# Kernel optimization log

Hardware: AMD Instinct MI355X
Metric: run time of the kernel (lower is better)

The kernel has to match this reference:

```python
import jax, jax.numpy as jnp
import numpy as np

N_NODES = 100000

def _sage_conv(x, edge_index, w_l, b_l, w_r):
    # PyG SAGEConv (mean aggr): out = lin_l(mean_j x_j) + lin_r(x)
    src, dst = edge_index[0], edge_index[1]
    msgs = x[src]  # [E, F] gather
    agg = jax.ops.segment_sum(msgs, dst, num_segments=N_NODES)
    cnt = jax.ops.segment_sum(jnp.ones((edge_index.shape[1],), x.dtype), dst, num_segments=N_NODES)
    agg = agg / jnp.maximum(cnt, 1.0)[:, None]  # mean; isolated nodes -> 0
    return agg @ w_l.T + b_l + x @ w_r.T

def setup_inputs() -> dict:
    key = jax.random.key(0)
    k = jax.random.split(key, 8)
    in_c, hid, out_c = 128, 64, 32
    x = jax.random.normal(k[0], (N_NODES, in_c), dtype=jnp.float32)
    edge_index = jax.random.randint(k[1], (2, 600000), 0, N_NODES, dtype=jnp.int64)
    s = lambda kk, fo, fi: jax.random.normal(kk, (fo, fi), jnp.float32) / jnp.sqrt(fi)
    return {
        'x': x,
        'edge_index': edge_index,
        'w1_l': s(k[2], hid, in_c),
        'b1_l': jnp.zeros((hid,), jnp.float32),
        'w1_r': s(k[3], hid, in_c),
        'w2_l': s(k[4], out_c, hid),
        'b2_l': jnp.zeros((out_c,), jnp.float32),
        'w2_r': s(k[5], out_c, hid),
    }

def reference(x, edge_index, w1_l, b1_l, w1_r, w2_l, b2_l, w2_r):
    h = _sage_conv(x, edge_index, w1_l, b1_l, w1_r)
    h = jax.nn.relu(h)
    # dropout(p=0.3) is identity in eval mode
    return _sage_conv(h, edge_index, w2_l, b2_l, w2_r)
```

## Files before the change

### kernel.cpp

```cpp
#include <hip/hip_runtime.h>

#define N_NODES 100000
#define N_EDGES 600000
#define N_PAD   100352
#define CAP     40
#define G1_TILES 3125
#define G1_TPB   5
#define G1_BLOCKS 625
#define CSR_EPT 17
#define CSR_EPB (CSR_EPT * 256)
#define CSR_BLOCKS 138
#define FRONT_BLOCKS (G1_BLOCKS + CSR_BLOCKS)
#define MID_BLOCKS 3125

typedef __bf16 bf16x8 __attribute__((ext_vector_type(8)));
typedef float  f32x4  __attribute__((ext_vector_type(4)));
typedef unsigned short u16x8 __attribute__((ext_vector_type(8)));
typedef unsigned short u16x4 __attribute__((ext_vector_type(4)));

__device__ inline unsigned short f2bf(float f) {
    __bf16 h = (__bf16)f;
    return __builtin_bit_cast(unsigned short, h);
}
__device__ inline float bf2f(unsigned short u) {
    return __builtin_bit_cast(float, ((unsigned)u) << 16);
}
__device__ inline bf16x8 ldfrag_bf16(const unsigned short* p) {
    u16x8 v = *(const u16x8*)p;
    return __builtin_bit_cast(bf16x8, v);
}

__global__ __launch_bounds__(256) void prep(
    const float* __restrict__ w1l, const float* __restrict__ w1r,
    const float* __restrict__ w2l, const float* __restrict__ w2r,
    unsigned short* __restrict__ wbf1, unsigned short* __restrict__ wbf2,
    int* __restrict__ deg)
{
    int i = blockIdx.x * 256 + threadIdx.x;
    deg[i] = 0;
    if (i < 16384) {
        int row = i >> 7, k = i & 127;
        float v = (row < 64) ? w1l[(row << 7) + k] : w1r[((row - 64) << 7) + k];
        wbf1[i] = f2bf(v);
    } else if (i < 20480) {
        int j = i - 16384;
        int row = j >> 6, k = j & 63;
        float v = (row < 32) ? w2l[(row << 6) + k] : w2r[((row - 32) << 6) + k];
        wbf2[j] = f2bf(v);
    }
}

__global__ __launch_bounds__(256) void front(
    const float* __restrict__ x,
    const unsigned short* __restrict__ wbf1,
    const int* __restrict__ ei,
    unsigned short* __restrict__ xl,
    unsigned short* __restrict__ xr,
    int* __restrict__ deg,
    int* __restrict__ csr32)
{
    const int b   = blockIdx.x;
    const int tid = threadIdx.x;

    if (b >= G1_BLOCKS) {
        const int cb = b - G1_BLOCKS;
        const int e0 = cb * CSR_EPB + tid;
        int dst[CSR_EPT], src[CSR_EPT];
        #pragma unroll
        for (int rr = 0; rr < CSR_EPT; ++rr) {
            int e = e0 + rr * 256;
            if (e < N_EDGES) { dst[rr] = ei[N_EDGES + e]; src[rr] = ei[e]; }
            else             { dst[rr] = -1; }
        }
        #pragma unroll
        for (int rr = 0; rr < CSR_EPT; ++rr) {
            if (dst[rr] >= 0) {
                int pos = atomicAdd(&deg[dst[rr]], 1);
                if (pos < CAP) csr32[dst[rr] * CAP + pos] = src[rr];
            }
        }
        return;
    }

    __shared__ unsigned short wlds[128 * 128];
    __shared__ unsigned short xs[2][32 * 128];

    #pragma unroll
    for (int i = 0; i < 8; ++i) {
        int idx = i * 256 + tid;
        int row = idx >> 4;
        int off = (idx & 15) << 4;
        u16x8 v = *(const u16x8*)(wbf1 + row * 128 + (off >> 1));
        *(u16x8*)((char*)wlds + row * 256 + (off ^ ((row & 7) << 4))) = v;
    }

    const int t0 = b * G1_TPB;

    const int wv   = tid >> 6;
    const int l    = tid & 63;
    const int lrow = l & 15;
    const int hi   = l >> 4;
    const int sr0  = tid >> 4;
    const int soff = (tid & 15) << 4;

    float4 pf[4];

    #define SLOAD(t) do {                                                      \
        _Pragma("unroll")                                                      \
        for (int rr = 0; rr < 2; ++rr) {                                       \
            const float* src = x + (size_t)((t) * 32 + sr0 + rr * 16) * 128    \
                                 + (soff >> 1);                                \
            pf[2*rr]   = *(const float4*)src;                                  \
            pf[2*rr+1] = *(const float4*)(src + 4);                            \
        }                                                                      \
    } while (0)

    #define SWRITE(bf) do {                                                    \
        _Pragma("unroll")                                                      \
        for (int rr = 0; rr < 2; ++rr) {                                       \
            int row = sr0 + rr * 16;                                           \
            u16x8 o;                                                           \
            o[0]=f2bf(pf[2*rr].x);   o[1]=f2bf(pf[2*rr].y);                    \
            o[2]=f2bf(pf[2*rr].z);   o[3]=f2bf(pf[2*rr].w);                    \
            o[4]=f2bf(pf[2*rr+1].x); o[5]=f2bf(pf[2*rr+1].y);                  \
            o[6]=f2bf(pf[2*rr+1].z); o[7]=f2bf(pf[2*rr+1].w);                  \
            *(u16x8*)((char*)&xs[bf][0] + row * 256                            \
                      + (soff ^ ((row & 7) << 4))) = o;                        \
        }                                                                      \
    } while (0)

    SLOAD(t0);
    SWRITE(0);
    __syncthreads();

    for (int tt = 0; tt < G1_TPB; ++tt) {
        if (tt + 1 < G1_TPB) SLOAD(t0 + tt + 1);

        char* xb = (char*)&xs[tt & 1][0];
        f32x4 acc[2][2];
        #pragma unroll
        for (int nt = 0; nt < 2; ++nt)
            #pragma unroll
            for (int ft = 0; ft < 2; ++ft) acc[nt][ft] = (f32x4){0.f,0.f,0.f,0.f};

        #pragma unroll
        for (int kt = 0; kt < 4; ++kt) {
            const int koff = kt * 64 + hi * 16;
            const int r0 = lrow, r1 = 16 + lrow;
            bf16x8 b0 = __builtin_bit_cast(bf16x8, *(const u16x8*)
                (xb + r0 * 256 + (koff ^ ((r0 & 7) << 4))));
            bf16x8 b1 = __builtin_bit_cast(bf16x8, *(const u16x8*)
                (xb + r1 * 256 + (koff ^ ((r1 & 7) << 4))));
            #pragma unroll
            for (int ft = 0; ft < 2; ++ft) {
                const int fr = wv * 32 + ft * 16 + lrow;
                bf16x8 a = __builtin_bit_cast(bf16x8, *(const u16x8*)
                    ((char*)wlds + fr * 256 + (koff ^ ((fr & 7) << 4))));
                acc[0][ft] = __builtin_amdgcn_mfma_f32_16x16x32_bf16(a, b0, acc[0][ft], 0, 0, 0);
                acc[1][ft] = __builtin_amdgcn_mfma_f32_16x16x32_bf16(a, b1, acc[1][ft], 0, 0, 0);
            }
        }

        if (tt + 1 < G1_TPB) SWRITE((tt + 1) & 1);
        __syncthreads();

        #pragma unroll
        for (int nt = 0; nt < 2; ++nt) {
            const int node = nt * 16 + lrow;
            #pragma unroll
            for (int ft = 0; ft < 2; ++ft) {
                const int fb = (wv * 32 + ft * 16 + hi * 4) * 2;
                u16x4 p;
                p[0] = f2bf(acc[nt][ft][0]); p[1] = f2bf(acc[nt][ft][1]);
                p[2] = f2bf(acc[nt][ft][2]); p[3] = f2bf(acc[nt][ft][3]);
                *(u16x4*)(xb + node * 256 + (fb ^ ((node & 7) << 4))) = p;
            }
        }
        __syncthreads();

        const int nbase = (t0 + tt) * 32;
        #pragma unroll
        for (int rr = 0; rr < 2; ++rr) {
            int idx = rr * 256 + tid;
            int row = idx >> 4;
            int off = (idx & 15) << 4;
            u16x8 v = *(const u16x8*)(xb + row * 256 + (off ^ ((row & 7) << 4)));
            if (off < 128) *(u16x8*)&xl[(nbase + row) * 64 + (off >> 1)] = v;
            else           *(u16x8*)&xr[(nbase + row) * 64 + ((off - 128) >> 1)] = v;
        }
        __syncthreads();
    }
    #undef SLOAD
    #undef SWRITE
}

__global__ __launch_bounds__(256) void mid(
    const unsigned short* __restrict__ xl,
    const unsigned short* __restrict__ xr,
    const int* __restrict__ deg,
    const int* __restrict__ csr32,
    const float* __restrict__ b1l,
    const unsigned short* __restrict__ wbf2,
    unsigned short* __restrict__ hl,
    unsigned short* __restrict__ hr)
{
    __shared__ unsigned short hs[32 * 64];

    const int tid = threadIdx.x;
    const int nd  = tid >> 3;
    const int q   = tid & 7;
    const int node = blockIdx.x * 32 + nd;

    const int beg = node * CAP;
    const int dg  = min(deg[node], CAP);

    float acc[8] = {0.f,0.f,0.f,0.f,0.f,0.f,0.f,0.f};
    int i = 0;
    for (; i + 4 <= dg; i += 4) {
        int s0 = csr32[beg + i];
        int s1 = csr32[beg + i + 1];
        int s2 = csr32[beg + i + 2];
        int s3 = csr32[beg + i + 3];
        u16x8 v0 = *(const u16x8*)&xl[s0 * 64 + 8 * q];
        u16x8 v1 = *(const u16x8*)&xl[s1 * 64 + 8 * q];
        u16x8 v2 = *(const u16x8*)&xl[s2 * 64 + 8 * q];
        u16x8 v3 = *(const u16x8*)&xl[s3 * 64 + 8 * q];
        #pragma unroll
        for (int j = 0; j < 8; ++j)
            acc[j] += (bf2f(v0[j]) + bf2f(v1[j])) + (bf2f(v2[j]) + bf2f(v3[j]));
    }
    for (; i < dg; ++i) {
        int s = csr32[beg + i];
        u16x8 v = *(const u16x8*)&xl[s * 64 + 8 * q];
        #pragma unroll
        for (int j = 0; j < 8; ++j) acc[j] += bf2f(v[j]);
    }
    const float inv = 1.0f / (float)max(dg, 1);
    u16x8 rv = *(const u16x8*)&xr[node * 64 + 8 * q];
    float4 b0 = *(const float4*)&b1l[8 * q];
    float4 b1 = *(const float4*)&b1l[8 * q + 4];
    float bb[8] = {b0.x,b0.y,b0.z,b0.w,b1.x,b1.y,b1.z,b1.w};
    u16x8 hv;
    #pragma unroll
    for (int j = 0; j < 8; ++j) {
        float o = fmaf(acc[j], inv, bb[j]) + bf2f(rv[j]);
        hv[j] = f2bf(fmaxf(o, 0.f));
    }
    *(u16x8*)((char*)hs + nd * 128 + ((q * 16) ^ ((nd & 7) << 4))) = hv;
    __syncthreads();

    const int wv   = tid >> 6;
    const int l    = tid & 63;
    const int lrow = l & 15;
    const int hi   = l >> 4;

    f32x4 a0 = (f32x4){0.f,0.f,0.f,0.f};
    f32x4 a1 = (f32x4){0.f,0.f,0.f,0.f};
    #pragma unroll
    for (int kt = 0; kt < 2; ++kt) {
        const int kin = kt * 64 + hi * 16;
        bf16x8 bf0 = __builtin_bit_cast(bf16x8, *(const u16x8*)
            ((const char*)hs + lrow * 128 + (kin ^ ((lrow & 7) << 4))));
        bf16x8 bf1 = __builtin_bit_cast(bf16x8, *(const u16x8*)
            ((const char*)hs + (16 + lrow) * 128 + (kin ^ ((lrow & 7) << 4))));
        bf16x8 a = ldfrag_bf16(wbf2 + (wv * 16 + lrow) * 64 + kt * 32 + hi * 8);
        a0 = __builtin_amdgcn_mfma_f32_16x16x32_bf16(a, bf0, a0, 0, 0, 0);
        a1 = __builtin_amdgcn_mfma_f32_16x16x32_bf16(a, bf1, a1, 0, 0, 0);
    }
    __syncthreads();

    {
        const int c2 = (wv * 16 + hi * 4) * 2;
        u16x4 p0, p1;
        p0[0]=f2bf(a0[0]); p0[1]=f2bf(a0[1]); p0[2]=f2bf(a0[2]); p0[3]=f2bf(a0[3]);
        p1[0]=f2bf(a1[0]); p1[1]=f2bf(a1[1]); p1[2]=f2bf(a1[2]); p1[3]=f2bf(a1[3]);
        const int n0l = lrow, n1l = 16 + lrow;
        *(u16x4*)((char*)hs + n0l * 128 + (c2 ^ ((n0l & 7) << 4))) = p0;
        *(u16x4*)((char*)hs + n1l * 128 + (c2 ^ ((n1l & 7) << 4))) = p1;
    }
    __syncthreads();

    {
        const int row = tid >> 3;
        const int off = (tid & 7) << 4;
        u16x8 v = *(const u16x8*)((char*)hs + row * 128 + (off ^ ((row & 7) << 4)));
        const int gn = blockIdx.x * 32 + row;
        if (off < 64) *(u16x8*)&hl[gn * 32 + (off >> 1)] = v;
        else          *(u16x8*)&hr[gn * 32 + ((off - 64) >> 1)] = v;
    }
}

__global__ __launch_bounds__(256) void gather2(
    const unsigned short* __restrict__ hl,
    const int* __restrict__ deg,
    const int* __restrict__ csr32,
    const float* __restrict__ b2l,
    const unsigned short* __restrict__ hr,
    float* __restrict__ out)
{
    int t = blockIdx.x * 256 + threadIdx.x;
    int n = t >> 2;
    int q = t & 3;
    if (n >= N_NODES) return;
    int beg = n * CAP, dg = min(deg[n], CAP);

    float acc[8] = {0.f,0.f,0.f,0.f,0.f,0.f,0.f,0.f};
    int i = 0;
    for (; i + 4 <= dg; i += 4) {
        int s0 = csr32[beg + i];
        int s1 = csr32[beg + i + 1];
        int s2 = csr32[beg + i + 2];
        int s3 = csr32[beg + i + 3];
        u16x8 v0 = *(const u16x8*)&hl[s0 * 32 + 8 * q];
        u16x8 v1 = *(const u16x8*)&hl[s1 * 32 + 8 * q];
        u16x8 v2 = *(const u16x8*)&hl[s2 * 32 + 8 * q];
        u16x8 v3 = *(const u16x8*)&hl[s3 * 32 + 8 * q];
        #pragma unroll
        for (int j = 0; j < 8; ++j)
            acc[j] += (bf2f(v0[j]) + bf2f(v1[j])) + (bf2f(v2[j]) + bf2f(v3[j]));
    }
    for (; i < dg; ++i) {
        int s = csr32[beg + i];
        u16x8 v = *(const u16x8*)&hl[s * 32 + 8 * q];
        #pragma unroll
        for (int j = 0; j < 8; ++j) acc[j] += bf2f(v[j]);
    }
    float inv = 1.0f / (float)max(dg, 1);
    u16x8 rv = *(const u16x8*)&hr[n * 32 + 8 * q];
    float4 b0 = *(const float4*)&b2l[8 * q];
    float4 b1 = *(const float4*)&b2l[8 * q + 4];
    float bb[8] = {b0.x,b0.y,b0.z,b0.w,b1.x,b1.y,b1.z,b1.w};
    float o[8];
    #pragma unroll
    for (int j = 0; j < 8; ++j)
        o[j] = fmaf(acc[j], inv, bb[j]) + bf2f(rv[j]);
    float* op = out + n * 32 + 8 * q;
    *(float4*)op       = make_float4(o[0], o[1], o[2], o[3]);
    *(float4*)(op + 4) = make_float4(o[4], o[5], o[6], o[7]);
}

extern "C" void kernel_launch(void* const* d_in, const int* in_sizes, int n_in,
                              void* d_out, int out_size, void* d_ws, size_t ws_size,
                              hipStream_t stream)
{
    const float* x   = (const float*)d_in[0];
    const int*   ei  = (const int*)d_in[1];
    const float* w1l = (const float*)d_in[2];
    const float* b1l = (const float*)d_in[3];
    const float* w1r = (const float*)d_in[4];
    const float* w2l = (const float*)d_in[5];
    const float* b2l = (const float*)d_in[6];
    const float* w2r = (const float*)d_in[7];
    float* out = (float*)d_out;

    char* ws = (char*)d_ws;
    unsigned short* xl   = (unsigned short*)(ws + 0);
    unsigned short* xr   = (unsigned short*)(ws + 12800000);
    unsigned short* hl   = (unsigned short*)(ws + 25600000);
    unsigned short* hr   = (unsigned short*)(ws + 32000000);
    int* csr32 = (int*)(ws + 38400000);
    int* deg   = (int*)(ws + 54400000);
    unsigned short* wbf1 = (unsigned short*)(ws + 54801408);
    unsigned short* wbf2 = (unsigned short*)(ws + 54834176);

    prep<<<392, 256, 0, stream>>>(w1l, w1r, w2l, w2r, wbf1, wbf2, deg);
    front<<<FRONT_BLOCKS, 256, 0, stream>>>(x, wbf1, ei, xl, xr, deg, csr32);
    mid<<<MID_BLOCKS, 256, 0, stream>>>(xl, xr, deg, csr32, b1l, wbf2, hl, hr);
    gather2<<<(N_NODES * 4 + 255) / 256, 256, 0, stream>>>(hl, deg, csr32, b2l, hr, out);
}
```

Baseline: 78.42 us.

## Split CSR build out of fused front kernel and vectorize edge loads

The fused front kernel, whose blocks did either the edge-bucketing CSR build or the first GEMM, is split into two separate launches: a build kernel and a gemm1 kernel. The build kernel now gives each thread 16 consecutive edges and reads them with int4 vector loads instead of strided scalar loads. This is meant to cut per-block register and LDS pressure, since CSR blocks no longer carry the GEMM's shared memory, and to widen memory transactions. In exchange it gives up overlapping the atomic-heavy build with the GEMM, and the build's loads are no longer coalesced across threads within a block.

```diff
diff --git a/kernel.cpp b/kernel.cpp
--- a/kernel.cpp
+++ b/kernel.cpp
@@ -7,10 +7,9 @@
 #define G1_TILES 3125
 #define G1_TPB   5
 #define G1_BLOCKS 625
-#define CSR_EPT 17
-#define CSR_EPB (CSR_EPT * 256)
-#define CSR_BLOCKS 138
-#define FRONT_BLOCKS (G1_BLOCKS + CSR_BLOCKS)
+#define BUILD_EPT 16
+#define BUILD_EPB (BUILD_EPT * 256)
+#define BUILD_BLOCKS 147
 #define MID_BLOCKS 3125
 
 typedef __bf16 bf16x8 __attribute__((ext_vector_type(8)));
@@ -50,37 +49,48 @@
     }
 }
 
-__global__ __launch_bounds__(256) void front(
+__global__ __launch_bounds__(256) void build(
+    const int* __restrict__ ei,
+    int* __restrict__ deg,
+    int* __restrict__ csr32)
+{
+    const int e0 = (blockIdx.x * 256 + threadIdx.x) * BUILD_EPT;
+    if (e0 >= N_EDGES) return;
+    int dst[BUILD_EPT], src[BUILD_EPT];
+    #pragma unroll
+    for (int c = 0; c < BUILD_EPT / 4; ++c) {
+        int e = e0 + c * 4;
+        if (e + 3 < N_EDGES) {
+            int4 d4 = *(const int4*)&ei[N_EDGES + e];
+            int4 s4 = *(const int4*)&ei[e];
+            dst[c*4+0] = d4.x; dst[c*4+1] = d4.y; dst[c*4+2] = d4.z; dst[c*4+3] = d4.w;
+            src[c*4+0] = s4.x; src[c*4+1] = s4.y; src[c*4+2] = s4.z; src[c*4+3] = s4.w;
+        } else {
+            #pragma unroll
+            for (int j = 0; j < 4; ++j) {
+                int ee = e + j;
+                if (ee < N_EDGES) { dst[c*4+j] = ei[N_EDGES + ee]; src[c*4+j] = ei[ee]; }
+                else              { dst[c*4+j] = -1; }
+            }
+        }
+    }
+    #pragma unroll
+    for (int r = 0; r < BUILD_EPT; ++r) {
+        if (dst[r] >= 0) {
+            int pos = atomicAdd(&deg[dst[r]], 1);
+            if (pos < CAP) csr32[dst[r] * CAP + pos] = src[r];
+        }
+    }
+}
+
+__global__ __launch_bounds__(256) void gemm1(
     const float* __restrict__ x,
     const unsigned short* __restrict__ wbf1,
-    const int* __restrict__ ei,
     unsigned short* __restrict__ xl,
-    unsigned short* __restrict__ xr,
-    int* __restrict__ deg,
-    int* __restrict__ csr32)
+    unsigned short* __restrict__ xr)
 {
     const int b   = blockIdx.x;
     const int tid = threadIdx.x;
-
-    if (b >= G1_BLOCKS) {
-        const int cb = b - G1_BLOCKS;
-        const int e0 = cb * CSR_EPB + tid;
-        int dst[CSR_EPT], src[CSR_EPT];
-        #pragma unroll
-        for (int rr = 0; rr < CSR_EPT; ++rr) {
-            int e = e0 + rr * 256;
-            if (e < N_EDGES) { dst[rr] = ei[N_EDGES + e]; src[rr] = ei[e]; }
-            else             { dst[rr] = -1; }
-        }
-        #pragma unroll
-        for (int rr = 0; rr < CSR_EPT; ++rr) {
-            if (dst[rr] >= 0) {
-                int pos = atomicAdd(&deg[dst[rr]], 1);
-                if (pos < CAP) csr32[dst[rr] * CAP + pos] = src[rr];
-            }
-        }
-        return;
-    }
 
     __shared__ unsigned short wlds[128 * 128];
     __shared__ unsigned short xs[2][32 * 128];
@@ -364,7 +374,8 @@
     unsigned short* wbf2 = (unsigned short*)(ws + 54834176);
 
     prep<<<392, 256, 0, stream>>>(w1l, w1r, w2l, w2r, wbf1, wbf2, deg);
-    front<<<FRONT_BLOCKS, 256, 0, stream>>>(x, wbf1, ei, xl, xr, deg, csr32);
+    build<<<BUILD_BLOCKS, 256, 0, stream>>>(ei, deg, csr32);
+    gemm1<<<G1_BLOCKS, 256, 0, stream>>>(x, wbf1, xl, xr);
     mid<<<MID_BLOCKS, 256, 0, stream>>>(xl, xr, deg, csr32, b1l, wbf2, hl, hr);
     gather2<<<(N_NODES * 4 + 255) / 256, 256, 0, stream>>>(hl, deg, csr32, b2l, hr, out);
 }
```

Result: slower. 87.60 us (+11.7%).
